# Kernel optimization log

Hardware: AMD Instinct MI355X
Metric: run time of the kernel (lower is better)

## Reference

```python
import jax, jax.numpy as jnp
import numpy as np

LORA_SCALE = 1.0 / 4.0  # alpha=1, rank=4
TAU_IOU = 0.1


def lora(x, W, A, B):
    # x @ W.T + (x @ A.T) @ B.T * scaling
    return x @ W.T + (x @ A.T) @ B.T * LORA_SCALE


def decode(h, Wd1, bd1, Wd2, bd2):
    # mask_decoder: Linear(embed,64) -> ReLU -> Linear(64,1)
    return (jax.nn.relu(h @ Wd1.T + bd1) @ Wd2.T + bd2)[..., 0]


def setup_inputs() -> dict:
    key = jax.random.key(0)
    ks = jax.random.split(key, 16)
    B, N, I, E, R = 2, 8192, 32, 128, 4
    s = lambda k, shape, f=0.05: jax.random.normal(k, shape, dtype=jnp.float32) * f
    return {
        "points": jax.random.normal(ks[0], (B, N, 3), dtype=jnp.float32),
        "pos_coords": jax.random.normal(ks[1], (B, I, 3), dtype=jnp.float32),
        "W1": s(ks[2], (64, 3), 0.3),
        "A1": s(ks[3], (R, 3), 0.3),
        "B1": s(ks[4], (64, R), 0.3),
        "W2": s(ks[5], (E, 64), 0.1),
        "A2": s(ks[6], (R, 64), 0.1),
        "B2": s(ks[7], (E, R), 0.1),
        "Wp": s(ks[8], (E, 3), 0.3),
        "bp": s(ks[9], (E,), 0.1),
        "Wd1": s(ks[10], (64, E), 0.1),
        "bd1": s(ks[11], (64,), 0.1),
        "Wd2": s(ks[12], (1, 64), 0.1),
        "bd2": s(ks[13], (1,), 0.1),
    }


def npc_neg_coords(initial_logits, pos_coords, key):
    # Vectorized replacement of the double python loop: for each (b,i),
    # uniformly sample one j with iou[b,i,j] >= tau (Gumbel-max trick);
    # if none, leave zeros.
    B, I, N = initial_logits.shape
    masks = (jax.nn.sigmoid(initial_logits) > 0.5).astype(initial_logits.dtype)  # [B,I,N]
    inter = jnp.einsum("bin,bjn->bij", masks, masks)
    m_sum = masks.sum(axis=2)  # [B,I]
    union = m_sum[:, :, None] + m_sum[:, None, :] - inter
    iou = inter / (union + 1e-6)
    iou = iou * (1.0 - jnp.eye(I, dtype=iou.dtype))  # zero diagonal
    cand = iou >= TAU_IOU  # [B,I,I]
    gumbel = -jnp.log(-jnp.log(jax.random.uniform(key, cand.shape, minval=1e-20, maxval=1.0)))
    scores = jnp.where(cand, gumbel, -jnp.inf)
    idx = jnp.argmax(scores, axis=-1)  # [B,I]
    valid = cand.any(axis=-1)  # [B,I]
    picked = jnp.take_along_axis(pos_coords, idx[..., None], axis=1)  # [B,I,3]
    return jnp.where(valid[..., None], picked, 0.0)


def reference(points, pos_coords, W1, A1, B1, W2, A2, B2, Wp, bp, Wd1, bd1, Wd2, bd2):
    # encoder: LoRA(3->64) -> ReLU -> LoRA(64->128)
    point_feats = lora(jax.nn.relu(lora(points, W1, A1, B1)), W2, A2, B2)  # [B,N,E]
    pos_embed = pos_coords @ Wp.T + bp  # [B,I,E]
    # [B,I,N,E] combined features
    initial_logits = decode(point_feats[:, None, :, :] + pos_embed[:, :, None, :], Wd1, bd1, Wd2, bd2)  # [B,I,N]
    neg_coords = npc_neg_coords(initial_logits, pos_coords, jax.random.key(42))
    neg_embed = neg_coords @ Wp.T + bp  # [B,I,E]
    refined_logits = decode(
        point_feats[:, None, :, :] + (pos_embed - neg_embed)[:, :, None, :], Wd1, bd1, Wd2, bd2
    )  # [B,I,N]
    return refined_logits, point_feats
```

## Files before the change

kernel.cpp:

```cpp
#include <hip/hip_runtime.h>

#define B_  2
#define N_  8192
#define I_  32
#define E_  128
#define H_  64
#define BN_ (B_*N_)
#define NW_ (N_/64)

typedef unsigned long long u64;

__device__ float g_pe  [B_*I_*E_];
__device__ float g_v1  [B_*I_*H_];
__device__ float g_v2  [B_*I_*H_];
__device__ float g_wd1t[E_*H_];
__device__ float g_u   [H_*BN_];
__device__ u64   g_masks[B_*I_*NW_];

__device__ __forceinline__ unsigned rotl_(unsigned x, unsigned n){ return (x<<n)|(x>>(32u-n)); }

__device__ void threefry_42(unsigned x0, unsigned x1, unsigned* r0, unsigned* r1){
  const unsigned ks0 = 0u, ks1 = 42u, ks2 = 0x1BD11BDAu ^ 0u ^ 42u;
  x0 += ks0; x1 += ks1;
  x0+=x1; x1=rotl_(x1,13); x1^=x0;
  x0+=x1; x1=rotl_(x1,15); x1^=x0;
  x0+=x1; x1=rotl_(x1,26); x1^=x0;
  x0+=x1; x1=rotl_(x1, 6); x1^=x0;
  x0+=ks1; x1+=ks2+1u;
  x0+=x1; x1=rotl_(x1,17); x1^=x0;
  x0+=x1; x1=rotl_(x1,29); x1^=x0;
  x0+=x1; x1=rotl_(x1,16); x1^=x0;
  x0+=x1; x1=rotl_(x1,24); x1^=x0;
  x0+=ks2; x1+=ks0+2u;
  x0+=x1; x1=rotl_(x1,13); x1^=x0;
  x0+=x1; x1=rotl_(x1,15); x1^=x0;
  x0+=x1; x1=rotl_(x1,26); x1^=x0;
  x0+=x1; x1=rotl_(x1, 6); x1^=x0;
  x0+=ks0; x1+=ks1+3u;
  x0+=x1; x1=rotl_(x1,17); x1^=x0;
  x0+=x1; x1=rotl_(x1,29); x1^=x0;
  x0+=x1; x1=rotl_(x1,16); x1^=x0;
  x0+=x1; x1=rotl_(x1,24); x1^=x0;
  x0+=ks1; x1+=ks2+4u;
  x0+=x1; x1=rotl_(x1,13); x1^=x0;
  x0+=x1; x1=rotl_(x1,15); x1^=x0;
  x0+=x1; x1=rotl_(x1,26); x1^=x0;
  x0+=x1; x1=rotl_(x1, 6); x1^=x0;
  x0+=ks2; x1+=ks0+5u;
  *r0 = x0; *r1 = x1;
}

__device__ float jax_uniform_2048(int e){
  unsigned o0, o1;
  threefry_42(0u, (unsigned)e, &o0, &o1);
  unsigned bits = o0 ^ o1;
  float u = __uint_as_float((bits >> 9) | 0x3f800000u) - 1.0f;
  u = u + 1e-20f;
  return fmaxf(1e-20f, u);
}

__global__ void __launch_bounds__(256) prep_kernel(
    const float* __restrict__ pos_coords,
    const float* __restrict__ Wp, const float* __restrict__ bp,
    const float* __restrict__ Wd1,const float* __restrict__ bd1)
{
  __shared__ float t_l [E_*65];
  __shared__ float pe_l[E_];
  const int row = blockIdx.x;
  const int tid = threadIdx.x;

  for (int idx = tid; idx < H_*E_; idx += 256){
    int k = idx >> 7, e = idx & 127;
    t_l[e*65 + k] = Wd1[idx];
  }
  if (tid < E_){
    const int e = tid;
    float s = pos_coords[row*3+0] * Wp[e*3+0];
    s = fmaf(pos_coords[row*3+1], Wp[e*3+1], s);
    s = fmaf(pos_coords[row*3+2], Wp[e*3+2], s);
    const float pe = s + bp[e];
    g_pe[row*E_ + e] = pe;
    pe_l[e] = pe;
  }
  __syncthreads();

  if (row == 0){
    for (int idx = tid; idx < E_*H_; idx += 256){
      int e = idx >> 6, k = idx & 63;
      g_wd1t[idx] = t_l[e*65 + k];
    }
  }
  if (tid < H_){
    const int k = tid;
    float s = 0.f;
    for (int e = 0; e < 128; ++e)
      s = fmaf(pe_l[e], t_l[e*65 + k], s);
    g_v1[row*H_ + k] = s + bd1[k];
  }
}

__global__ void __launch_bounds__(512) enc_kernel(
    const float* __restrict__ points,
    const float* __restrict__ W1, const float* __restrict__ A1,
    const float* __restrict__ B1, const float* __restrict__ W2,
    const float* __restrict__ A2, const float* __restrict__ B2,
    const float* __restrict__ Wd2,const float* __restrict__ bd2,
    float* __restrict__ out_pf)
{
  __shared__ float pf_l  [E_*65];
  __shared__ float u_l   [64*65];
  __shared__ float w2_l  [E_*H_];
  __shared__ float wd1t_l[E_*H_];
  const int tid  = threadIdx.x;
  const int w_u  = __builtin_amdgcn_readfirstlane(tid >> 6);
  const int lane = tid & 63;
  const int p0   = blockIdx.x * 64;
  const int p    = p0 + lane;
  const int b    = blockIdx.x >> 7;

  for (int idx = tid; idx < E_*H_; idx += 512){
    w2_l[idx]   = W2[idx];
    wd1t_l[idx] = g_wd1t[idx];
  }

  const float x0 = points[p*3+0];
  const float x1 = points[p*3+1];
  const float x2 = points[p*3+2];

  float a1[4];
  #pragma unroll
  for (int r = 0; r < 4; ++r){
    float s = x0 * A1[r*3+0];
    s = fmaf(x1, A1[r*3+1], s);
    s = fmaf(x2, A1[r*3+2], s);
    a1[r] = s;
  }
  float t1[64];
  #pragma unroll
  for (int k = 0; k < 64; ++k){
    float s = x0 * W1[k*3+0];
    s = fmaf(x1, W1[k*3+1], s);
    s = fmaf(x2, W1[k*3+2], s);
    float l = a1[0] * B1[k*4+0];
    l = fmaf(a1[1], B1[k*4+1], l);
    l = fmaf(a1[2], B1[k*4+2], l);
    l = fmaf(a1[3], B1[k*4+3], l);
    t1[k] = fmaxf(fmaf(0.25f, l, s), 0.0f);
  }
  float a2[4];
  #pragma unroll
  for (int r = 0; r < 4; ++r){
    float s = 0.f;
    #pragma unroll
    for (int j = 0; j < 64; ++j) s = fmaf(t1[j], A2[r*64+j], s);
    a2[r] = s;
  }
  __syncthreads();

  const int e0 = w_u * 16;
  for (int ei = 0; ei < 16; ++ei){
    const int e = e0 + ei;
    const float* w2row = w2_l + e*64;
    float s1 = 0.f;
    #pragma unroll
    for (int j = 0; j < 64; ++j) s1 = fmaf(t1[j], w2row[j], s1);
    float s2 = a2[0] * B2[e*4+0];
    s2 = fmaf(a2[1], B2[e*4+1], s2);
    s2 = fmaf(a2[2], B2[e*4+2], s2);
    s2 = fmaf(a2[3], B2[e*4+3], s2);
    pf_l[e*65 + lane] = fmaf(0.25f, s2, s1);
  }
  __syncthreads();

  const int kbase = w_u * 8;
  float uacc[8];
  #pragma unroll
  for (int kk = 0; kk < 8; ++kk) uacc[kk] = 0.f;
  for (int e = 0; e < 128; ++e){
    const float pf = pf_l[e*65 + lane];
    const float* wrow = wd1t_l + e*64 + kbase;
    #pragma unroll
    for (int kk = 0; kk < 8; ++kk)
      uacc[kk] = fmaf(pf, wrow[kk], uacc[kk]);
  }
  #pragma unroll
  for (int kk = 0; kk < 8; ++kk){
    g_u[(size_t)(kbase + kk) * BN_ + p] = uacc[kk];
    u_l[lane*65 + kbase + kk] = uacc[kk];
  }
  __syncthreads();

  for (int idx = tid; idx < 64*E_; idx += 512){
    const int pt = idx >> 7, e = idx & 127;
    out_pf[(size_t)p0 * E_ + idx] = pf_l[e*65 + pt];
  }

  const float bd2v = bd2[0];
  float acc[4];
  #pragma unroll
  for (int ii = 0; ii < 4; ++ii) acc[ii] = 0.f;
  const int ibase = w_u * 4;
  const float* v = g_v1 + ((b * I_ + ibase) << 6);
  for (int k = 0; k < 64; ++k){
    const float wd2k = Wd2[k];
    const float uk = u_l[lane*65 + k];
    #pragma unroll
    for (int ii = 0; ii < 4; ++ii)
      acc[ii] = fmaf(wd2k, fmaxf(uk + v[ii*64 + k], 0.0f), acc[ii]);
  }
  #pragma unroll
  for (int ii = 0; ii < 4; ++ii){
    const int i = ibase + ii;
    u64 bal = __ballot(acc[ii] + bd2v > 0.0f);
    if (lane == 0) g_masks[(size_t)(b * I_ + i) * NW_ + (blockIdx.x & 127)] = bal;
  }
}

__global__ void __launch_bounds__(256) sample_kernel(
    const float* __restrict__ pos_coords,
    const float* __restrict__ Wp, const float* __restrict__ bp,
    const float* __restrict__ bd1)
{
  __shared__ int   inter_l[4*32];
  __shared__ int   msum_l[32];
  __shared__ float delta_l[4*E_];
  __shared__ float nc_l[4][3];
  const int tid  = threadIdx.x;
  const int row0 = blockIdx.x * 4;
  const int b    = row0 >> 5;

  {
    const int pair = tid >> 1;
    const int rl   = pair >> 5;
    const int j    = pair & 31;
    const int half = tid & 1;
    const u64* mi = g_masks + (size_t)(row0 + rl) * NW_ + half*64;
    const u64* mj = g_masks + (size_t)(b*32 + j)  * NW_ + half*64;
    int s = 0;
    #pragma unroll
    for (int w = 0; w < 64; ++w) s += __popcll(mi[w] & mj[w]);
    s += __shfl_xor(s, 1, 64);
    if (half == 0) inter_l[pair] = s;
  }
  {
    const int j  = tid >> 3;
    const int ws = (tid & 7) * 16;
    const u64* mj = g_masks + (size_t)(b*32 + j) * NW_;
    int s = 0;
    #pragma unroll
    for (int w = 0; w < 16; ++w) s += __popcll(mj[ws + w]);
    s += __shfl_xor(s, 1, 64);
    s += __shfl_xor(s, 2, 64);
    s += __shfl_xor(s, 4, 64);
    if ((tid & 7) == 0) msum_l[j] = s;
  }
  __syncthreads();

  if (tid < 4){
    const int row = row0 + tid;
    const int i = row & 31;
    const int msum_i = msum_l[i];
    float best = -INFINITY; int bestj = 0; bool any = false;
    for (int j = 0; j < 32; ++j){
      const int inter = inter_l[(tid << 5) + j];
      const int uni   = msum_i + msum_l[j] - inter;
      const float iou = (float)inter / ((float)uni + 1e-6f);
      const bool cand = (j != i) && (iou >= 0.1f);
      if (cand){
        any = true;
        const float uu = jax_uniform_2048((row << 5) + j);
        const float g  = -logf(-logf(uu));
        if (g > best){ best = g; bestj = j; }
      }
    }
    nc_l[tid][0] = any ? pos_coords[(b*32 + bestj)*3 + 0] : 0.f;
    nc_l[tid][1] = any ? pos_coords[(b*32 + bestj)*3 + 1] : 0.f;
    nc_l[tid][2] = any ? pos_coords[(b*32 + bestj)*3 + 2] : 0.f;
  }
  __syncthreads();

  for (int idx = tid; idx < 4*E_; idx += 256){
    const int rl = idx >> 7, e = idx & 127;
    float ne = nc_l[rl][0] * Wp[e*3+0];
    ne = fmaf(nc_l[rl][1], Wp[e*3+1], ne);
    ne = fmaf(nc_l[rl][2], Wp[e*3+2], ne);
    ne = ne + bp[e];
    delta_l[idx] = g_pe[(row0 + rl)*E_ + e] - ne;
  }
  __syncthreads();

  {
    const int rl = tid >> 6, k = tid & 63;
    float s = 0.f;
    for (int e = 0; e < 128; ++e)
      s = fmaf(delta_l[rl*E_ + e], g_wd1t[e*64 + k], s);
    g_v2[(row0 + rl)*H_ + k] = s + bd1[k];
  }
}

__global__ void __launch_bounds__(1024) dec_kernel(
    const float* __restrict__ Wd2, const float* __restrict__ bd2,
    float* __restrict__ out0)
{
  __shared__ float u_l[64*65];
  const int tid  = threadIdx.x;
  const int w_u  = __builtin_amdgcn_readfirstlane(tid >> 6);
  const int lane = tid & 63;
  const int bc   = blockIdx.x;
  const int b    = bc >> 7;
  const int nb   = (bc & 127) << 6;
  const int n    = nb + lane;

  for (int idx = tid; idx < 64*64; idx += 1024){
    const int k = idx >> 6, pl = idx & 63;
    u_l[pl*65 + k] = g_u[(size_t)k * BN_ + b * N_ + nb + pl];
  }
  __syncthreads();

  const float bd2v = bd2[0];
  float acc[2];
  acc[0] = 0.f; acc[1] = 0.f;
  const int ibase = w_u * 2;
  const float* v = g_v2 + ((b * I_ + ibase) << 6);
  for (int k = 0; k < 64; ++k){
    const float wd2k = Wd2[k];
    const float uk = u_l[lane*65 + k];
    acc[0] = fmaf(wd2k, fmaxf(uk + v[k],      0.0f), acc[0]);
    acc[1] = fmaf(wd2k, fmaxf(uk + v[64 + k], 0.0f), acc[1]);
  }
  #pragma unroll
  for (int ii = 0; ii < 2; ++ii){
    const int i = ibase + ii;
    out0[(size_t)(b * I_ + i) * N_ + n] = acc[ii] + bd2v;
  }
}

extern "C" void kernel_launch(void* const* d_in, const int* in_sizes, int n_in,
                              void* d_out, int out_size, void* d_ws, size_t ws_size,
                              hipStream_t stream)
{
  (void)in_sizes; (void)n_in; (void)out_size; (void)d_ws; (void)ws_size;
  const float* points     = (const float*)d_in[0];
  const float* pos_coords = (const float*)d_in[1];
  const float* W1  = (const float*)d_in[2];
  const float* A1  = (const float*)d_in[3];
  const float* B1  = (const float*)d_in[4];
  const float* W2  = (const float*)d_in[5];
  const float* A2  = (const float*)d_in[6];
  const float* B2  = (const float*)d_in[7];
  const float* Wp  = (const float*)d_in[8];
  const float* bp  = (const float*)d_in[9];
  const float* Wd1 = (const float*)d_in[10];
  const float* bd1 = (const float*)d_in[11];
  const float* Wd2 = (const float*)d_in[12];
  const float* bd2 = (const float*)d_in[13];

  float* out0   = (float*)d_out;
  float* out_pf = out0 + (size_t)B_ * I_ * N_;

  prep_kernel<<<64, 256, 0, stream>>>(pos_coords, Wp, bp, Wd1, bd1);
  enc_kernel<<<256, 512, 0, stream>>>(points, W1, A1, B1, W2, A2, B2,
                                      Wd2, bd2, out_pf);
  sample_kernel<<<16, 256, 0, stream>>>(pos_coords, Wp, bp, bd1);
  dec_kernel<<<256, 1024, 0, stream>>>(Wd2, bd2, out0);
}
```

Baseline: 145.1 us.

## Fold LoRA adapters into effective weights and precompose W2·Wd1 in prep kernel

The prep kernel gains an extra block that merges each LoRA's low-rank update into an effective weight matrix (W1eff, W2eff). It also precomputes the product M = W2eff^T·Wd1^T, so the encoder computes the decoder hidden projection u directly from t1 (64-deep) instead of from point_feats (128-deep). This removes the per-point rank-4 adapter work and halves the inner dot length of the u computation, and it also drops one barrier. The cost is a small serial GEMM in one prep block and a different floating-point summation order.

```diff
diff --git a/kernel.cpp b/kernel.cpp
--- a/kernel.cpp
+++ b/kernel.cpp
@@ -16,6 +16,9 @@
 __device__ float g_wd1t[E_*H_];
 __device__ float g_u   [H_*BN_];
 __device__ u64   g_masks[B_*I_*NW_];
+__device__ float g_w1eff[H_*3];
+__device__ float g_w2eff[E_*H_];
+__device__ float g_meff [H_*H_];
 
 __device__ __forceinline__ unsigned rotl_(unsigned x, unsigned n){ return (x<<n)|(x>>(32u-n)); }
 
@@ -62,9 +65,13 @@
 __global__ void __launch_bounds__(256) prep_kernel(
     const float* __restrict__ pos_coords,
     const float* __restrict__ Wp, const float* __restrict__ bp,
-    const float* __restrict__ Wd1,const float* __restrict__ bd1)
+    const float* __restrict__ Wd1,const float* __restrict__ bd1,
+    const float* __restrict__ W1, const float* __restrict__ A1,
+    const float* __restrict__ B1, const float* __restrict__ W2,
+    const float* __restrict__ A2, const float* __restrict__ B2)
 {
   __shared__ float t_l [E_*65];
+  __shared__ float w2_l[E_*65];
   __shared__ float pe_l[E_];
   const int row = blockIdx.x;
   const int tid = threadIdx.x;
@@ -73,44 +80,82 @@
     int k = idx >> 7, e = idx & 127;
     t_l[e*65 + k] = Wd1[idx];
   }
-  if (tid < E_){
-    const int e = tid;
-    float s = pos_coords[row*3+0] * Wp[e*3+0];
-    s = fmaf(pos_coords[row*3+1], Wp[e*3+1], s);
-    s = fmaf(pos_coords[row*3+2], Wp[e*3+2], s);
-    const float pe = s + bp[e];
-    g_pe[row*E_ + e] = pe;
-    pe_l[e] = pe;
-  }
-  __syncthreads();
-
-  if (row == 0){
-    for (int idx = tid; idx < E_*H_; idx += 256){
-      int e = idx >> 6, k = idx & 63;
-      g_wd1t[idx] = t_l[e*65 + k];
-    }
-  }
-  if (tid < H_){
-    const int k = tid;
-    float s = 0.f;
-    for (int e = 0; e < 128; ++e)
-      s = fmaf(pe_l[e], t_l[e*65 + k], s);
-    g_v1[row*H_ + k] = s + bd1[k];
+
+  if (row < 64){
+    if (tid < E_){
+      const int e = tid;
+      float s = pos_coords[row*3+0] * Wp[e*3+0];
+      s = fmaf(pos_coords[row*3+1], Wp[e*3+1], s);
+      s = fmaf(pos_coords[row*3+2], Wp[e*3+2], s);
+      const float pe = s + bp[e];
+      g_pe[row*E_ + e] = pe;
+      pe_l[e] = pe;
+    }
+    __syncthreads();
+
+    if (row == 0){
+      for (int idx = tid; idx < E_*H_; idx += 256){
+        int e = idx >> 6, k = idx & 63;
+        g_wd1t[idx] = t_l[e*65 + k];
+      }
+    }
+    if (tid < H_){
+      const int k = tid;
+      float s = 0.f;
+      for (int e = 0; e < 128; ++e)
+        s = fmaf(pe_l[e], t_l[e*65 + k], s);
+      g_v1[row*H_ + k] = s + bd1[k];
+    }
+    return;
+  }
+
+  for (int idx = tid; idx < E_*H_; idx += 256){
+    const int e = idx >> 6, j = idx & 63;
+    float l = B2[e*4+0] * A2[0*64+j];
+    l = fmaf(B2[e*4+1], A2[1*64+j], l);
+    l = fmaf(B2[e*4+2], A2[2*64+j], l);
+    l = fmaf(B2[e*4+3], A2[3*64+j], l);
+    const float v = fmaf(0.25f, l, W2[idx]);
+    w2_l[e*65 + j] = v;
+    g_w2eff[idx] = v;
+  }
+  if (tid < H_*3){
+    const int k = tid / 3, c = tid % 3;
+    float l = B1[k*4+0] * A1[0*3+c];
+    l = fmaf(B1[k*4+1], A1[1*3+c], l);
+    l = fmaf(B1[k*4+2], A1[2*3+c], l);
+    l = fmaf(B1[k*4+3], A1[3*3+c], l);
+    g_w1eff[tid] = fmaf(0.25f, l, W1[tid]);
+  }
+  __syncthreads();
+
+  {
+    const int j  = tid >> 2;
+    const int kq = tid & 3;
+    float acc[16];
+    #pragma unroll
+    for (int kk = 0; kk < 16; ++kk) acc[kk] = 0.f;
+    for (int e = 0; e < E_; ++e){
+      const float w = w2_l[e*65 + j];
+      #pragma unroll
+      for (int kk = 0; kk < 16; ++kk)
+        acc[kk] = fmaf(w, t_l[e*65 + kq*16 + kk], acc[kk]);
+    }
+    #pragma unroll
+    for (int kk = 0; kk < 16; ++kk)
+      g_meff[j*64 + kq*16 + kk] = acc[kk];
   }
 }
 
 __global__ void __launch_bounds__(512) enc_kernel(
     const float* __restrict__ points,
-    const float* __restrict__ W1, const float* __restrict__ A1,
-    const float* __restrict__ B1, const float* __restrict__ W2,
-    const float* __restrict__ A2, const float* __restrict__ B2,
-    const float* __restrict__ Wd2,const float* __restrict__ bd2,
+    const float* __restrict__ Wd2, const float* __restrict__ bd2,
     float* __restrict__ out_pf)
 {
-  __shared__ float pf_l  [E_*65];
-  __shared__ float u_l   [64*65];
-  __shared__ float w2_l  [E_*H_];
-  __shared__ float wd1t_l[E_*H_];
+  __shared__ float pf_l[E_*65];
+  __shared__ float u_l [64*65];
+  __shared__ float w2_l[E_*H_];
+  __shared__ float me_l[H_*H_];
   const int tid  = threadIdx.x;
   const int w_u  = __builtin_amdgcn_readfirstlane(tid >> 6);
   const int lane = tid & 63;
@@ -118,70 +163,56 @@
   const int p    = p0 + lane;
   const int b    = blockIdx.x >> 7;
 
-  for (int idx = tid; idx < E_*H_; idx += 512){
-    w2_l[idx]   = W2[idx];
-    wd1t_l[idx] = g_wd1t[idx];
-  }
+  for (int idx = tid; idx < E_*H_; idx += 512) w2_l[idx] = g_w2eff[idx];
+  for (int idx = tid; idx < H_*H_; idx += 512) me_l[idx] = g_meff[idx];
 
   const float x0 = points[p*3+0];
   const float x1 = points[p*3+1];
   const float x2 = points[p*3+2];
 
-  float a1[4];
-  #pragma unroll
-  for (int r = 0; r < 4; ++r){
-    float s = x0 * A1[r*3+0];
-    s = fmaf(x1, A1[r*3+1], s);
-    s = fmaf(x2, A1[r*3+2], s);
-    a1[r] = s;
-  }
   float t1[64];
   #pragma unroll
   for (int k = 0; k < 64; ++k){
-    float s = x0 * W1[k*3+0];
-    s = fmaf(x1, W1[k*3+1], s);
-    s = fmaf(x2, W1[k*3+2], s);
-    float l = a1[0] * B1[k*4+0];
-    l = fmaf(a1[1], B1[k*4+1], l);
-    l = fmaf(a1[2], B1[k*4+2], l);
-    l = fmaf(a1[3], B1[k*4+3], l);
-    t1[k] = fmaxf(fmaf(0.25f, l, s), 0.0f);
-  }
-  float a2[4];
-  #pragma unroll
-  for (int r = 0; r < 4; ++r){
-    float s = 0.f;
-    #pragma unroll
-    for (int j = 0; j < 64; ++j) s = fmaf(t1[j], A2[r*64+j], s);
-    a2[r] = s;
+    float s = x0 * g_w1eff[k*3+0];
+    s = fmaf(x1, g_w1eff[k*3+1], s);
+    s = fmaf(x2, g_w1eff[k*3+2], s);
+    t1[k] = fmaxf(s, 0.0f);
   }
   __syncthreads();
 
   const int e0 = w_u * 16;
   for (int ei = 0; ei < 16; ++ei){
     const int e = e0 + ei;
-    const float* w2row = w2_l + e*64;
+    const float4* w2row = (const float4*)(w2_l + e*64);
     float s1 = 0.f;
     #pragma unroll
-    for (int j = 0; j < 64; ++j) s1 = fmaf(t1[j], w2row[j], s1);
-    float s2 = a2[0] * B2[e*4+0];
-    s2 = fmaf(a2[1], B2[e*4+1], s2);
-    s2 = fmaf(a2[2], B2[e*4+2], s2);
-    s2 = fmaf(a2[3], B2[e*4+3], s2);
-    pf_l[e*65 + lane] = fmaf(0.25f, s2, s1);
-  }
-  __syncthreads();
+    for (int j4 = 0; j4 < 16; ++j4){
+      const float4 w = w2row[j4];
+      s1 = fmaf(t1[j4*4+0], w.x, s1);
+      s1 = fmaf(t1[j4*4+1], w.y, s1);
+      s1 = fmaf(t1[j4*4+2], w.z, s1);
+      s1 = fmaf(t1[j4*4+3], w.w, s1);
+    }
+    pf_l[e*65 + lane] = s1;
+  }
 
   const int kbase = w_u * 8;
   float uacc[8];
   #pragma unroll
   for (int kk = 0; kk < 8; ++kk) uacc[kk] = 0.f;
-  for (int e = 0; e < 128; ++e){
-    const float pf = pf_l[e*65 + lane];
-    const float* wrow = wd1t_l + e*64 + kbase;
-    #pragma unroll
-    for (int kk = 0; kk < 8; ++kk)
-      uacc[kk] = fmaf(pf, wrow[kk], uacc[kk]);
+  #pragma unroll 4
+  for (int j = 0; j < 64; ++j){
+    const float t = t1[j];
+    const float4 m0 = *(const float4*)(me_l + j*64 + kbase);
+    const float4 m1 = *(const float4*)(me_l + j*64 + kbase + 4);
+    uacc[0] = fmaf(t, m0.x, uacc[0]);
+    uacc[1] = fmaf(t, m0.y, uacc[1]);
+    uacc[2] = fmaf(t, m0.z, uacc[2]);
+    uacc[3] = fmaf(t, m0.w, uacc[3]);
+    uacc[4] = fmaf(t, m1.x, uacc[4]);
+    uacc[5] = fmaf(t, m1.y, uacc[5]);
+    uacc[6] = fmaf(t, m1.z, uacc[6]);
+    uacc[7] = fmaf(t, m1.w, uacc[7]);
   }
   #pragma unroll
   for (int kk = 0; kk < 8; ++kk){
@@ -358,9 +389,9 @@
   float* out0   = (float*)d_out;
   float* out_pf = out0 + (size_t)B_ * I_ * N_;
 
-  prep_kernel<<<64, 256, 0, stream>>>(pos_coords, Wp, bp, Wd1, bd1);
-  enc_kernel<<<256, 512, 0, stream>>>(points, W1, A1, B1, W2, A2, B2,
-                                      Wd2, bd2, out_pf);
+  prep_kernel<<<65, 256, 0, stream>>>(pos_coords, Wp, bp, Wd1, bd1,
+                                      W1, A1, B1, W2, A2, B2);
+  enc_kernel<<<256, 512, 0, stream>>>(points, Wd2, bd2, out_pf);
   sample_kernel<<<16, 256, 0, stream>>>(pos_coords, Wp, bp, bd1);
   dec_kernel<<<256, 1024, 0, stream>>>(Wd2, bd2, out0);
 }
```

Result: slower. 160.0 us (+10.3%).
